# Performance work log

Hardware: AMD Instinct MI355X
Metric: run time of the kernel (lower is better)

Reference implementation:

```python
import jax, jax.numpy as jnp
import numpy as np

TAPS = 5
DELAY = 3
EPS_POWER = 1e-7   # clamp for inverse power (wpe_one_iteration eps)
EPS_REG = 1e-10    # diagonal loading of the correlation matrix


def setup_inputs() -> dict:
    key = jax.random.key(0)
    ks = jax.random.split(key, 5)
    B, F, C, T = 8, 257, 8, 800
    shp = (B, F, C, T)
    return {
        "data_sep_real": jax.random.normal(ks[0], shp, jnp.float32),
        "data_sep_imag": jax.random.normal(ks[1], shp, jnp.float32),
        "data_mix_real": jax.random.normal(ks[2], shp, jnp.float32),
        "data_mix_imag": jax.random.normal(ks[3], shp, jnp.float32),
        "ilens": jax.random.randint(ks[4], (B,), 1, T + 1, jnp.int32),
    }


def _ytilde(Y, taps, delay):
    # Y: (B,F,C,T) complex -> stacked delayed taps (B,F,taps*C,T)
    # tap k at time t holds Y[..., t - delay - k] (zero-padded past)
    B, F, C, T = Y.shape
    Yp = jnp.pad(Y, ((0, 0), (0, 0), (0, 0), (delay + taps - 1, 0)))
    tilde = jnp.stack(
        [Yp[..., taps - 1 - k: taps - 1 - k + T] for k in range(taps)], axis=2
    )  # (B,F,taps,C,T)
    return tilde.reshape(B, F, taps * C, T)


def _wpe_one_iteration(Y, power, taps, delay):
    # Y: (B,F,C,T) complex, power: (B,F,T) real
    B, F, C, T = Y.shape
    inv_power = 1.0 / jnp.maximum(power, EPS_POWER)          # (B,F,T)
    Yt = _ytilde(Y, taps, delay)                              # (B,F,K,T), K=taps*C
    t0 = delay + taps - 1                                     # correlations use t >= t0
    Ytv = Yt[..., t0:]
    Yv = Y[..., t0:]
    Ytw = Ytv * inv_power[:, :, None, t0:].astype(Y.dtype)
    # R = sum_t w(t) Ytilde(t) Ytilde(t)^H  -> (B,F,K,K)
    R = jnp.einsum('bfat,bfct->bfac', Ytw, jnp.conj(Ytv))
    # P = sum_t w(t) Ytilde(t) Y(t)^H      -> (B,F,K,C)
    P = jnp.einsum('bfat,bfet->bfae', Ytw, jnp.conj(Yv))
    K = taps * C
    R = R + EPS_REG * jnp.eye(K, dtype=R.dtype)
    G = jnp.linalg.solve(R, P)                                # (B,F,K,C)
    # X(t) = Y(t) - G^H Ytilde(t)
    X = Y - jnp.einsum('bfae,bfat->bfet', jnp.conj(G), Yt)
    return X


def reference(data_sep_real, data_sep_imag, data_mix_real, data_mix_imag, ilens):
    # power of separated signal, averaged over channels (use_dnn_mask=False)
    power = jnp.mean(data_sep_real ** 2 + data_sep_imag ** 2, axis=-2)  # (B,F,T)
    Ym = jax.lax.complex(data_mix_real, data_mix_imag)                  # (B,F,C,T)
    X = _wpe_one_iteration(Ym, power, TAPS, DELAY)
    # zero out padded frames: t >= ilens[b]
    t = jnp.arange(X.shape[-1])
    valid = t[None, :] < ilens[:, None]                                 # (B,T)
    X = jnp.where(valid[:, None, None, :], X, 0)
    # return real/imag stacked on last axis: (B,F,C,T,2)
    return jnp.stack([X.real, X.imag], axis=-1)
```

## Files before the change

kernel.cpp:

```cpp
#include <hip/hip_runtime.h>

#define B 8
#define F 257
#define C 8
#define T 800
#define TAPS 5
#define DELAY 3
#define K 40
#define NCOL 48
#define T0 7
#define BF (B*F)

typedef __bf16 bf16x8 __attribute__((ext_vector_type(8)));
typedef __bf16 bf16x4 __attribute__((ext_vector_type(4)));
typedef float f32x4 __attribute__((ext_vector_type(4)));

struct PF { float4 v[3]; };

__global__ __launch_bounds__(256) void power_kernel(const float* __restrict__ sr,
                                                    const float* __restrict__ si,
                                                    float* __restrict__ W) {
    int bf = blockIdx.x;
    const float* srp = sr + (size_t)bf * C * T;
    const float* sip = si + (size_t)bf * C * T;
    int t0 = threadIdx.x * 4;
    if (t0 < T) {
        float s[4] = {0.f, 0.f, 0.f, 0.f};
#pragma unroll
        for (int c = 0; c < C; ++c) {
            float4 a = *(const float4*)(srp + c * T + t0);
            float4 b = *(const float4*)(sip + c * T + t0);
            s[0] = fmaf(a.x, a.x, fmaf(b.x, b.x, s[0]));
            s[1] = fmaf(a.y, a.y, fmaf(b.y, b.y, s[1]));
            s[2] = fmaf(a.z, a.z, fmaf(b.z, b.z, s[2]));
            s[3] = fmaf(a.w, a.w, fmaf(b.w, b.w, s[3]));
        }
        float4 w;
        float* wp = (float*)&w;
#pragma unroll
        for (int e = 0; e < 4; ++e) {
            float v = fmaxf(s[e] * (1.0f / C), 1e-7f);
            wp[e] = (t0 + e < T0) ? 0.f : rsqrtf(v);
        }
        *(float4*)(W + (size_t)bf * T + t0) = w;
    }
}

#define WB3 7680

__global__ __launch_bounds__(256, 3) void rp_mfma_kernel(const float* __restrict__ mr,
                                                         const float* __restrict__ mi,
                                                         const float* __restrict__ W,
                                                         float2* __restrict__ Rout,
                                                         float2* __restrict__ Pout) {
    __shared__ __align__(16) unsigned char SH[4 * WB3];
    const int lane = threadIdx.x & 63;
    const int wid = threadIdx.x >> 6;
    const int bf = blockIdx.x * 4 + wid;
    unsigned char* base = SH + wid * WB3;

    const float* mrp = mr + (size_t)bf * C * T;
    const float* mip = mi + (size_t)bf * C * T;
    const float* Wp  = W  + (size_t)bf * T;

    const int q = lane >> 4, col = lane & 15;
    const int pc = lane >> 3, pg = lane & 7;

    const int PM[6] = {0, 0, 0, 1, 1, 2};
    const int PN[6] = {0, 1, 2, 1, 2, 2};

    const float* ysr = mrp + pc * T + pg * 4 - 8;
    const float* ysi = mip + pc * T + pg * 4 - 8;
    const float* wsr = Wp + pg * 4;

    f32x4 accRe[6], accIr[6], accRi[6];
#pragma unroll
    for (int p = 0; p < 6; ++p) {
        accRe[p] = (f32x4){0.f, 0.f, 0.f, 0.f};
        accIr[p] = (f32x4){0.f, 0.f, 0.f, 0.f};
        accRi[p] = (f32x4){0.f, 0.f, 0.f, 0.f};
    }

    float4 yr0, yr1, yr2, yi0, yi1, yi2, wcur;
    {
        const float* cbr = mrp + pc * T;
        const float* cbi = mip + pc * T;
        bool h0 = (pg < 2), h1 = (pg < 1);
        yr0 = *(const float4*)(h0 ? cbr : ysr);
        yr1 = *(const float4*)(h1 ? cbr : (ysr + 4));
        yr2 = *(const float4*)(ysr + 8);
        yi0 = *(const float4*)(h0 ? cbi : ysi);
        yi1 = *(const float4*)(h1 ? cbi : (ysi + 4));
        yi2 = *(const float4*)(ysi + 8);
        wcur = *(const float4*)wsr;
        if (h0) { yr0 = make_float4(0.f,0.f,0.f,0.f); yi0 = make_float4(0.f,0.f,0.f,0.f); }
        if (h1) { yr1 = make_float4(0.f,0.f,0.f,0.f); yi1 = make_float4(0.f,0.f,0.f,0.f); }
    }

    for (int ks = 0; ks < 25; ++ks) {
        {
            float yre[12], yim[12];
            yre[0] = yr0.x; yre[1] = yr0.y; yre[2]  = yr0.z; yre[3]  = yr0.w;
            yre[4] = yr1.x; yre[5] = yr1.y; yre[6]  = yr1.z; yre[7]  = yr1.w;
            yre[8] = yr2.x; yre[9] = yr2.y; yre[10] = yr2.z; yre[11] = yr2.w;
            yim[0] = yi0.x; yim[1] = yi0.y; yim[2]  = yi0.z; yim[3]  = yi0.w;
            yim[4] = yi1.x; yim[5] = yi1.y; yim[6]  = yi1.z; yim[7]  = yi1.w;
            yim[8] = yi2.x; yim[9] = yi2.y; yim[10] = yi2.z; yim[11] = yi2.w;
            float wv[4] = {wcur.x, wcur.y, wcur.z, wcur.w};
#pragma unroll
            for (int v = 0; v < 6; ++v) {
                int row = (v < 5) ? (v * 8 + pc) : (40 + pc);
                int off = (v < 5) ? (5 - v) : 8;
                bf16x4 zr, zi;
#pragma unroll
                for (int e = 0; e < 4; ++e) {
                    zr[e] = (__bf16)(wv[e] * yre[off + e]);
                    zi[e] = (__bf16)(wv[e] * yim[off + e]);
                }
                *(bf16x4*)(base + row * 80 + pg * 8) = zr;
                *(bf16x4*)(base + 3840 + row * 80 + pg * 8) = zi;
            }
        }

        float4 nyr0, nyr1, nyr2, nyi0, nyi1, nyi2, nw;
        if (ks < 24) {
            int off = (ks + 1) * 32;
            nyr0 = *(const float4*)(ysr + off);
            nyr1 = *(const float4*)(ysr + off + 4);
            nyr2 = *(const float4*)(ysr + off + 8);
            nyi0 = *(const float4*)(ysi + off);
            nyi1 = *(const float4*)(ysi + off + 4);
            nyi2 = *(const float4*)(ysi + off + 8);
            nw   = *(const float4*)(wsr + off);
        }

        bf16x8 fr[3], fi[3];
#pragma unroll
        for (int X = 0; X < 3; ++X) {
            fr[X] = *(const bf16x8*)(base + (X * 16 + col) * 80 + q * 16);
            fi[X] = *(const bf16x8*)(base + 3840 + (X * 16 + col) * 80 + q * 16);
        }
#pragma unroll
        for (int p = 0; p < 6; ++p) {
            int mt = PM[p], nt = PN[p];
            accRe[p] = __builtin_amdgcn_mfma_f32_16x16x32_bf16(fr[mt], fr[nt], accRe[p], 0, 0, 0);
            accRe[p] = __builtin_amdgcn_mfma_f32_16x16x32_bf16(fi[mt], fi[nt], accRe[p], 0, 0, 0);
            accIr[p] = __builtin_amdgcn_mfma_f32_16x16x32_bf16(fi[mt], fr[nt], accIr[p], 0, 0, 0);
            accRi[p] = __builtin_amdgcn_mfma_f32_16x16x32_bf16(fr[mt], fi[nt], accRi[p], 0, 0, 0);
        }

        if (ks < 24) {
            yr0 = nyr0; yr1 = nyr1; yr2 = nyr2;
            yi0 = nyi0; yi1 = nyi1; yi2 = nyi2;
            wcur = nw;
        }
    }

    float2* Rp = Rout + (size_t)bf * K * K;
    float2* Pp = Pout + (size_t)bf * K * C;
#pragma unroll
    for (int p = 0; p < 6; ++p) {
        int mt = PM[p], nt = PN[p];
#pragma unroll
        for (int r = 0; r < 4; ++r) {
            int m = mt * 16 + q * 4 + r;
            int n = nt * 16 + col;
            float re = accRe[p][r];
            float im = accIr[p][r] - accRi[p][r];
            if (m < K) {
                if (n < K) {
                    if (m == n) re += 1e-10f;
                    Rp[m * K + n] = make_float2(re, im);
                } else {
                    Pp[m * C + (n - K)] = make_float2(re, im);
                }
            }
            if (mt != nt && m < K && n < K)
                Rp[n * K + m] = make_float2(re, -im);
        }
    }
}

__device__ __forceinline__ float rdlane(float v, int j) {
    return __uint_as_float(__builtin_amdgcn_readlane(__float_as_uint(v), (unsigned)j));
}

__global__ __launch_bounds__(256) void solve_kernel(const float2* __restrict__ Rin,
                                                    const float2* __restrict__ Pin,
                                                    float2* __restrict__ Gout) {
    __shared__ float2 lbuf[2][64];
    const int bf = blockIdx.x;
    const int lane = threadIdx.x & 63;
    const int w = threadIdx.x >> 6;
    const bool act = lane < K;
    const int lr = act ? lane : 0;

    float2 colw[12];
    {
        const float2* Arow = Rin + (size_t)bf * K * K + (size_t)lr * K;
        const float2* Prow = Pin + (size_t)bf * K * C + (size_t)lr * C;
#pragma unroll
        for (int m = 0; m < 10; ++m) {
            float2 v = Arow[4 * m + w];
            colw[m] = act ? v : make_float2(0.f, 0.f);
        }
#pragma unroll
        for (int m = 10; m < 12; ++m) {
            float2 v = Prow[4 * (m - 10) + w];
            colw[m] = act ? v : make_float2(0.f, 0.f);
        }
    }

#pragma unroll
    for (int j = 0; j < K; ++j) {
        const int par = j & 1;
        const int wo = j & 3;
        const int mj = j >> 2;
        if (w == wo) {
            float dx = rdlane(colw[mj].x, j);
            float dy = rdlane(colw[mj].y, j);
            float den = fmaf(dx, dx, dy * dy);
            float r = 1.0f / den;
            float ix = dx * r, iy = -dy * r;
            float lx = colw[mj].x * ix - colw[mj].y * iy;
            float ly = colw[mj].x * iy + colw[mj].y * ix;
            bool isj = (lane == j);
            lx = isj ? (1.0f - ix) : lx;
            ly = isj ? (0.0f - iy) : ly;
            lbuf[par][lane] = make_float2(lx, ly);
        }
        __syncthreads();
        float2 l = lbuf[par][lane];
#pragma unroll
        for (int m = 0; m < 12; ++m) {
            if (4 * m + 3 <= j) continue;
            bool doit = (4 * m > j) || (4 * m + w > j);
            if (doit) {
                float ux = rdlane(colw[m].x, j);
                float uy = rdlane(colw[m].y, j);
                colw[m].x = fmaf(-l.x, ux, fmaf( l.y, uy, colw[m].x));
                colw[m].y = fmaf(-l.x, uy, fmaf(-l.y, ux, colw[m].y));
            }
        }
    }

    if (act) {
        float2* Gp = Gout + (size_t)bf * K * C + (size_t)lane * C;
        Gp[w]     = colw[10];
        Gp[4 + w] = colw[11];
    }
}

#define XSTR 144
#define XWB 12032

__device__ __forceinline__ PF x_load(const float* __restrict__ mrp,
                                     const float* __restrict__ mip,
                                     int tb, int lane) {
    PF p;
#pragma unroll
    for (int it = 0; it < 3; ++it) {
        int task = lane + it * 64;
        float4 v = make_float4(0.f, 0.f, 0.f, 0.f);
        if (task < 160) {
            int pl = task / 80;
            int rem = task - pl * 80;
            int c = rem / 10, grp = rem - c * 10;
            int tg = tb - 8 + grp * 4;
            const float* srcp = pl ? mip : mrp;
            if (tg >= 0) v = *(const float4*)(srcp + c * T + tg);
        }
        p.v[it] = v;
    }
    return p;
}

__device__ __forceinline__ void x_store(const PF& p, float* sre, float* sim_, int lane) {
#pragma unroll
    for (int it = 0; it < 3; ++it) {
        int task = lane + it * 64;
        if (task < 160) {
            int pl = task / 80;
            int rem = task - pl * 80;
            int c = rem / 10, grp = rem - c * 10;
            *(float4*)((pl ? sim_ : sre) + c * 44 + grp * 4) = p.v[it];
        }
    }
}

__global__ __launch_bounds__(256) void x_mfma_kernel(const float* __restrict__ mr,
                                                     const float* __restrict__ mi,
                                                     const float2* __restrict__ Gin,
                                                     const int* __restrict__ ilens,
                                                     float2* __restrict__ out) {
    __shared__ __align__(16) unsigned char SH[4 * XWB];
    const int lane = threadIdx.x & 63;
    const int split = threadIdx.x >> 6;
    const int bf = blockIdx.x;
    const int ck0 = (split == 0) ? 0 : (1 + split * 6);
    const int nck = (split == 0) ? 7 : 6;
    unsigned char* base = SH + split * XWB;
    float* sre = (float*)(base + 9216);
    float* sim_ = (float*)(base + 10624);

    const float* mrp = mr + (size_t)bf * C * T;
    const float* mip = mi + (size_t)bf * C * T;
    const float2* Gp = Gin + (size_t)bf * K * C;
    float2* outp = out + (size_t)bf * C * T;
    const int len = ilens[bf / F];

    const int q = lane >> 4, col = lane & 15;
    const int t2 = lane >> 1, half = lane & 1;

#pragma unroll
    for (int pl = 0; pl < 2; ++pl) {
        unsigned char* pb = base + pl * 4608 + t2 * XSTR + 80 + half * 24;
        *(float2*)(pb)      = make_float2(0.f, 0.f);
        *(float2*)(pb + 8)  = make_float2(0.f, 0.f);
        *(float2*)(pb + 16) = make_float2(0.f, 0.f);
    }

    bf16x8 Agr[2], Agi[2], Agin[2];
#pragma unroll
    for (int ks = 0; ks < 2; ++ks)
#pragma unroll
        for (int j = 0; j < 8; ++j) {
            int a = ks * 32 + q * 8 + j;
            float2 g = make_float2(0.f, 0.f);
            if (a < K && col < C) g = Gp[a * C + col];
            Agr[ks][j]  = (__bf16)g.x;
            Agi[ks][j]  = (__bf16)g.y;
            Agin[ks][j] = (__bf16)(-g.y);
        }

    PF cur = x_load(mrp, mip, ck0 * 32, lane);

    for (int ci = 0; ci < nck; ++ci) {
        const int tb = (ck0 + ci) * 32;

        x_store(cur, sre, sim_, lane);
        if (ci + 1 < nck) cur = x_load(mrp, mip, tb + 32, lane);

#pragma unroll
        for (int i = 0; i < 5; ++i) {
            int abase = half * 20 + 4 * i;
            bf16x4 zr, zi;
#pragma unroll
            for (int e2 = 0; e2 < 4; ++e2) {
                int a = abase + e2;
                int v = a >> 3, c = a & 7;
                int idx = c * 44 + t2 + 5 - v;
                zr[e2] = (__bf16)sre[idx];
                zi[e2] = (__bf16)sim_[idx];
            }
            *(bf16x4*)(base + t2 * XSTR + abase * 2) = zr;
            *(bf16x4*)(base + 4608 + t2 * XSTR + abase * 2) = zi;
        }

#pragma unroll
        for (int tt = 0; tt < 2; ++tt) {
            const int trow = tt * 16 + col;
            f32x4 accRe = (f32x4){0.f, 0.f, 0.f, 0.f};
            f32x4 accIm = (f32x4){0.f, 0.f, 0.f, 0.f};
#pragma unroll
            for (int ks = 0; ks < 2; ++ks) {
                bf16x8 byr = *(const bf16x8*)(base + trow * XSTR + ks * 64 + q * 16);
                bf16x8 byi = *(const bf16x8*)(base + 4608 + trow * XSTR + ks * 64 + q * 16);
                accRe = __builtin_amdgcn_mfma_f32_16x16x32_bf16(Agr[ks], byr, accRe, 0, 0, 0);
                accRe = __builtin_amdgcn_mfma_f32_16x16x32_bf16(Agi[ks], byi, accRe, 0, 0, 0);
                accIm = __builtin_amdgcn_mfma_f32_16x16x32_bf16(Agr[ks], byi, accIm, 0, 0, 0);
                accIm = __builtin_amdgcn_mfma_f32_16x16x32_bf16(Agin[ks], byr, accIm, 0, 0, 0);
            }
            if (q < 2) {
                int t = tb + tt * 16 + col;
                int l = tt * 16 + col + 8;
                bool ok = (t < len);
#pragma unroll
                for (int r = 0; r < 4; ++r) {
                    int e = q * 4 + r;
                    float yr = sre[e * 44 + l];
                    float yi = sim_[e * 44 + l];
                    float2 v = ok ? make_float2(yr - accRe[r], yi - accIm[r])
                                  : make_float2(0.f, 0.f);
                    outp[e * T + t] = v;
                }
            }
        }
    }
}

extern "C" void kernel_launch(void* const* d_in, const int* in_sizes, int n_in,
                              void* d_out, int out_size, void* d_ws, size_t ws_size,
                              hipStream_t stream) {
    const float* sep_r = (const float*)d_in[0];
    const float* sep_i = (const float*)d_in[1];
    const float* mix_r = (const float*)d_in[2];
    const float* mix_i = (const float*)d_in[3];
    const int* ilens   = (const int*)d_in[4];

    float* ws = (float*)d_ws;
    float* W = ws;
    float2* Rws = (float2*)(ws + (size_t)BF * T);
    float2* Gws = Rws + (size_t)BF * K * K;

    power_kernel<<<BF, 256, 0, stream>>>(sep_r, sep_i, W);
    rp_mfma_kernel<<<BF / 4, 256, 0, stream>>>(mix_r, mix_i, W, Rws, Gws);
    solve_kernel<<<BF, 256, 0, stream>>>(Rws, Gws, Gws);
    x_mfma_kernel<<<BF, 256, 0, stream>>>(mix_r, mix_i, Gws, ilens, (float2*)d_out);
}
```

Measured before the change: 153.8 us.

## Split R/P time reduction across two waves per frequency bin

The correlation kernel now gives each (b,f) two wavefronts, each covering half of the 25 time chunks. The partial accumulators are combined through shared memory before the even wave writes R and P. This doubles the grid so the GPU has more waves in flight and each wave runs a shorter serial chain, at the cost of extra LDS traffic and block-wide syncs for the reduction.

```diff
diff --git a/kernel.cpp b/kernel.cpp
--- a/kernel.cpp
+++ b/kernel.cpp
@@ -56,7 +56,10 @@
     __shared__ __align__(16) unsigned char SH[4 * WB3];
     const int lane = threadIdx.x & 63;
     const int wid = threadIdx.x >> 6;
-    const int bf = blockIdx.x * 4 + wid;
+    const int bf = blockIdx.x * 2 + (wid >> 1);
+    const int half = wid & 1;
+    const int ck0 = half ? 13 : 0;
+    const int nck = half ? 12 : 13;
     unsigned char* base = SH + wid * WB3;
 
     const float* mrp = mr + (size_t)bf * C * T;
@@ -82,7 +85,7 @@
     }
 
     float4 yr0, yr1, yr2, yi0, yi1, yi2, wcur;
-    {
+    if (half == 0) {
         const float* cbr = mrp + pc * T;
         const float* cbi = mip + pc * T;
         bool h0 = (pg < 2), h1 = (pg < 1);
@@ -95,9 +98,18 @@
         wcur = *(const float4*)wsr;
         if (h0) { yr0 = make_float4(0.f,0.f,0.f,0.f); yi0 = make_float4(0.f,0.f,0.f,0.f); }
         if (h1) { yr1 = make_float4(0.f,0.f,0.f,0.f); yi1 = make_float4(0.f,0.f,0.f,0.f); }
-    }
-
-    for (int ks = 0; ks < 25; ++ks) {
+    } else {
+        int o0 = ck0 * 32;
+        yr0 = *(const float4*)(ysr + o0);
+        yr1 = *(const float4*)(ysr + o0 + 4);
+        yr2 = *(const float4*)(ysr + o0 + 8);
+        yi0 = *(const float4*)(ysi + o0);
+        yi1 = *(const float4*)(ysi + o0 + 4);
+        yi2 = *(const float4*)(ysi + o0 + 8);
+        wcur = *(const float4*)(wsr + o0);
+    }
+
+    for (int ks = ck0; ks < ck0 + nck; ++ks) {
         {
             float yre[12], yim[12];
             yre[0] = yr0.x; yre[1] = yr0.y; yre[2]  = yr0.z; yre[3]  = yr0.w;
@@ -123,7 +135,7 @@
         }
 
         float4 nyr0, nyr1, nyr2, nyi0, nyi1, nyi2, nw;
-        if (ks < 24) {
+        if (ks + 1 < ck0 + nck) {
             int off = (ks + 1) * 32;
             nyr0 = *(const float4*)(ysr + off);
             nyr1 = *(const float4*)(ysr + off + 4);
@@ -149,34 +161,64 @@
             accRi[p] = __builtin_amdgcn_mfma_f32_16x16x32_bf16(fr[mt], fi[nt], accRi[p], 0, 0, 0);
         }
 
-        if (ks < 24) {
+        if (ks + 1 < ck0 + nck) {
             yr0 = nyr0; yr1 = nyr1; yr2 = nyr2;
             yi0 = nyi0; yi1 = nyi1; yi2 = nyi2;
             wcur = nw;
         }
     }
 
-    float2* Rp = Rout + (size_t)bf * K * K;
-    float2* Pp = Pout + (size_t)bf * K * C;
-#pragma unroll
-    for (int p = 0; p < 6; ++p) {
-        int mt = PM[p], nt = PN[p];
-#pragma unroll
-        for (int r = 0; r < 4; ++r) {
-            int m = mt * 16 + q * 4 + r;
-            int n = nt * 16 + col;
-            float re = accRe[p][r];
-            float im = accIr[p][r] - accRi[p][r];
-            if (m < K) {
-                if (n < K) {
-                    if (m == n) re += 1e-10f;
-                    Rp[m * K + n] = make_float2(re, im);
-                } else {
-                    Pp[m * C + (n - K)] = make_float2(re, im);
+    __syncthreads();
+    float* rbuf = (float*)SH;
+#pragma unroll
+    for (int pair = 0; pair < 2; ++pair) {
+        if (wid == pair * 2 + 1) {
+#pragma unroll
+            for (int p = 0; p < 6; ++p)
+#pragma unroll
+                for (int r = 0; r < 4; ++r) {
+                    rbuf[((p * 3 + 0) * 4 + r) * 64 + lane] = accRe[p][r];
+                    rbuf[((p * 3 + 1) * 4 + r) * 64 + lane] = accIr[p][r];
+                    rbuf[((p * 3 + 2) * 4 + r) * 64 + lane] = accRi[p][r];
                 }
-            }
-            if (mt != nt && m < K && n < K)
-                Rp[n * K + m] = make_float2(re, -im);
+        }
+        __syncthreads();
+        if (wid == pair * 2) {
+#pragma unroll
+            for (int p = 0; p < 6; ++p)
+#pragma unroll
+                for (int r = 0; r < 4; ++r) {
+                    accRe[p][r] += rbuf[((p * 3 + 0) * 4 + r) * 64 + lane];
+                    accIr[p][r] += rbuf[((p * 3 + 1) * 4 + r) * 64 + lane];
+                    accRi[p][r] += rbuf[((p * 3 + 2) * 4 + r) * 64 + lane];
+                }
+        }
+        __syncthreads();
+    }
+
+    if ((wid & 1) == 0) {
+        float2* Rp = Rout + (size_t)bf * K * K;
+        float2* Pp = Pout + (size_t)bf * K * C;
+#pragma unroll
+        for (int p = 0; p < 6; ++p) {
+            int mt = PM[p], nt = PN[p];
+#pragma unroll
+            for (int r = 0; r < 4; ++r) {
+                int m = mt * 16 + q * 4 + r;
+                int n = nt * 16 + col;
+                float re = accRe[p][r];
+                float im = accIr[p][r] - accRi[p][r];
+                if (m < K) {
+                    if (n < K) {
+                        if (m == n) re += 1e-10f;
+                        Rp[m * K + n] = make_float2(re, im);
+                    } else {
+                        Pp[m * C + (n - K)] = make_float2(re, im);
+                    }
+                }
+                if (mt != nt && m < K && n < K)
+                    Rp[n * K + m] = make_float2(re, -im);
+            }
         }
     }
 }
@@ -404,7 +446,7 @@
     float2* Gws = Rws + (size_t)BF * K * K;
 
     power_kernel<<<BF, 256, 0, stream>>>(sep_r, sep_i, W);
-    rp_mfma_kernel<<<BF / 4, 256, 0, stream>>>(mix_r, mix_i, W, Rws, Gws);
+    rp_mfma_kernel<<<BF / 2, 256, 0, stream>>>(mix_r, mix_i, W, Rws, Gws);
     solve_kernel<<<BF, 256, 0, stream>>>(Rws, Gws, Gws);
     x_mfma_kernel<<<BF, 256, 0, stream>>>(mix_r, mix_i, Gws, ilens, (float2*)d_out);
 }
```

Measured after the change: 153.5 us. About the same (-0.2%).
